# Performance work log

Hardware: AMD Instinct MI355X
Metric: run time of the kernel (lower is better)

Reference implementation:

```python
import jax, jax.numpy as jnp
import numpy as np

GRID_SIZE = 5       # efficient-KAN defaults
SPLINE_ORDER = 3
GRID_RANGE = (-1.0, 1.0)
N_BASIS = GRID_SIZE + SPLINE_ORDER  # 8
LN_EPS = 1e-5


def _make_grid(in_features):
    h = (GRID_RANGE[1] - GRID_RANGE[0]) / GRID_SIZE
    g = np.arange(-SPLINE_ORDER, GRID_SIZE + SPLINE_ORDER + 1, dtype=np.float32) * h + GRID_RANGE[0]
    return jnp.asarray(np.tile(g, (in_features, 1)))  # [in, G+2k+1]


def _b_splines(x, grid):
    # x: [N, in], grid: [in, G+2k+1] -> [N, in, G+k]
    x = x[..., None]
    bases = ((x >= grid[:, :-1]) & (x < grid[:, 1:])).astype(x.dtype)
    for k in range(1, SPLINE_ORDER + 1):
        bases = ((x - grid[:, : -(k + 1)]) / (grid[:, k:-1] - grid[:, : -(k + 1)]) * bases[..., :-1]
                 + (grid[:, k + 1:] - x) / (grid[:, k + 1:] - grid[:, 1:-k]) * bases[..., 1:])
    return bases


def _layer_norm(x, scale, bias):
    mu = jnp.mean(x, axis=-1, keepdims=True)
    var = jnp.mean(jnp.square(x - mu), axis=-1, keepdims=True)
    return (x - mu) * jax.lax.rsqrt(var + LN_EPS) * scale + bias


def setup_inputs() -> dict:
    key = jax.random.key(0)
    B, S, D = 2, 4096, 256
    IN = 3 * D
    ks = jax.random.split(key, 20)
    s = 0.02
    inp = {
        'axial_tokens': jax.random.normal(ks[0], (B, S, D), jnp.float32),
        'sagittal_tokens': jax.random.normal(ks[1], (B, S, D), jnp.float32),
        'coronal_tokens': jax.random.normal(ks[2], (B, S, D), jnp.float32),
        'wq': jax.random.normal(ks[3], (D, D), jnp.float32) * s,
        'bq': jnp.zeros((D,), jnp.float32),
        'wk': jax.random.normal(ks[4], (D, D), jnp.float32) * s,
        'bk': jnp.zeros((D,), jnp.float32),
        'wv': jax.random.normal(ks[5], (D, D), jnp.float32) * s,
        'bv': jnp.zeros((D,), jnp.float32),
        'view_emb': jax.random.normal(ks[6], (3, D), jnp.float32) * s,
        'ln_ax_scale': jnp.ones((D,), jnp.float32), 'ln_ax_bias': jnp.zeros((D,), jnp.float32),
        'ln_sg_scale': jnp.ones((D,), jnp.float32), 'ln_sg_bias': jnp.zeros((D,), jnp.float32),
        'ln_co_scale': jnp.ones((D,), jnp.float32), 'ln_co_bias': jnp.zeros((D,), jnp.float32),
        'base_weight': jax.random.normal(ks[7], (D, IN), jnp.float32) * s,
        'spline_weight': jax.random.normal(ks[8], (D, IN, N_BASIS), jnp.float32) * s,
        'spline_scaler': 1.0 + jax.random.normal(ks[9], (D, IN), jnp.float32) * 0.1,
    }
    return inp


def reference(axial_tokens, sagittal_tokens, coronal_tokens,
              wq, bq, wk, bk, wv, bv, view_emb,
              ln_ax_scale, ln_ax_bias, ln_sg_scale, ln_sg_bias, ln_co_scale, ln_co_bias,
              base_weight, spline_weight, spline_scaler):
    D = axial_tokens.shape[-1]
    inv_sqrt_d = 1.0 / jnp.sqrt(jnp.float32(D))

    def attend(tokens, emb, ln_s, ln_b):
        q = tokens @ wq.T + bq
        k = tokens @ wk.T + bk
        v = tokens @ wv.T + bv
        # torch adds q @ view_emb_row_broadcast^T: every column of the bias equals q . emb
        bias = (q @ emb)[..., None]                      # [B,S,1]
        scores = jnp.einsum('bqd,bkd->bqk', q, k) * inv_sqrt_d + bias
        w = jax.nn.softmax(scores, axis=-1)
        att = jnp.einsum('bqk,bkd->bqd', w, v)
        return _layer_norm(att + tokens, ln_s, ln_b)

    ax = attend(axial_tokens, view_emb[0], ln_ax_scale, ln_ax_bias)
    sg = attend(sagittal_tokens, view_emb[1], ln_sg_scale, ln_sg_bias)
    co = attend(coronal_tokens, view_emb[2], ln_co_scale, ln_co_bias)

    x = jnp.concatenate((ax, sg, co), axis=-1)          # [B,S,3D]
    B, S, IN = x.shape
    grid = _make_grid(IN)
    base = jax.nn.silu(x) @ base_weight.T               # [B,S,D]
    sb = _b_splines(x.reshape(-1, IN), grid)            # [B*S, IN, G+k]
    sw = spline_weight * spline_scaler[..., None]       # [D, IN, G+k]
    spline = jnp.einsum('nif,oif->no', sb, sw).reshape(B, S, -1)
    return base + spline
```

## Files before the change

### kernel.cpp

```cpp
#include <hip/hip_runtime.h>
#include <hip/hip_bf16.h>
#include <math.h>


typedef __hip_bfloat16 bf16;
using bf16x8 = __attribute__((ext_vector_type(8))) __bf16;
using f32x4  = __attribute__((ext_vector_type(4))) float;

__device__ __forceinline__ void load_lds16(const void* g, void* l) {
  __builtin_amdgcn_global_load_lds((__attribute__((address_space(1))) void*)g,
                                   (__attribute__((address_space(3))) void*)l,
                                   16, 0, 0);
}

__device__ __forceinline__ float wave_sum(float v) {
#pragma unroll
  for (int o = 32; o > 0; o >>= 1) v += __shfl_down(v, o, 64);
  return v;
}

template <typename OutT, bool EXP>
__global__ __launch_bounds__(256) void mfma_gemm_bt(
    const bf16* __restrict__ A, const bf16* __restrict__ B,
    const float* __restrict__ bias, OutT* __restrict__ C, int K, int lda,
    int ldb, int ldc, size_t zAh, size_t zAl, size_t zBh, size_t zBl,
    size_t zC, float scale) {
  __shared__ __align__(16) bf16 As[4096];
  __shared__ __align__(16) bf16 Bs[4096];
  const int tid = (int)threadIdx.x;
  const int lane = tid & 63;
  const int w = tid >> 6;
  const int m0 = (int)blockIdx.y << 7;
  const int n0 = (int)blockIdx.x << 7;
  const size_t z = blockIdx.z;
  A += (z >> 1) * zAh + (z & 1) * zAl;
  B += (z >> 1) * zBh + (z & 1) * zBl;
  C += z * zC;

  const int srow = lane >> 2;
  const int qg = (lane & 3) ^ ((lane >> 3) & 3);
  const int ci0 = w, ci1 = w + 4;
  const bf16* gA0 = A + (size_t)(m0 + ci0 * 16 + srow) * lda + qg * 8;
  const bf16* gA1 = A + (size_t)(m0 + ci1 * 16 + srow) * lda + qg * 8;
  const bf16* gB0 = B + (size_t)(n0 + ci0 * 16 + srow) * ldb + qg * 8;
  const bf16* gB1 = B + (size_t)(n0 + ci1 * 16 + srow) * ldb + qg * 8;
  bf16* lA0 = As + ci0 * 512;
  bf16* lA1 = As + ci1 * 512;
  bf16* lB0 = Bs + ci0 * 512;
  bf16* lB1 = Bs + ci1 * 512;

  const int m15 = lane & 15, quad = lane >> 4;
  const int fq = quad ^ ((m15 >> 1) & 3);
  const int aoff = m15 * 32 + fq * 8;
  const bf16* pA = As + ((w >> 1) << 11) + aoff;
  const bf16* pB = Bs + ((w & 1) << 11) + aoff;

  f32x4 acc[4][4];
#pragma unroll
  for (int mi = 0; mi < 4; ++mi)
#pragma unroll
    for (int ni = 0; ni < 4; ++ni) acc[mi][ni] = (f32x4)(0.0f);

  for (int k0 = 0; k0 < K; k0 += 32) {
    load_lds16(gA0, lA0);
    load_lds16(gA1, lA1);
    load_lds16(gB0, lB0);
    load_lds16(gB1, lB1);
    gA0 += 32; gA1 += 32; gB0 += 32; gB1 += 32;
    __syncthreads();
    bf16x8 av[4], bv[4];
#pragma unroll
    for (int i = 0; i < 4; ++i) {
      av[i] = *(const bf16x8*)(pA + i * 512);
      bv[i] = *(const bf16x8*)(pB + i * 512);
    }
#pragma unroll
    for (int mi = 0; mi < 4; ++mi)
#pragma unroll
      for (int ni = 0; ni < 4; ++ni)
        acc[mi][ni] = __builtin_amdgcn_mfma_f32_16x16x32_bf16(
            av[mi], bv[ni], acc[mi][ni], 0, 0, 0);
    __syncthreads();
  }

  const int crow = m0 + ((w >> 1) << 6) + quad * 4;
  const int ccol = n0 + ((w & 1) << 6) + m15;
#pragma unroll
  for (int ni = 0; ni < 4; ++ni) {
    const int col = ccol + ni * 16;
    const float bb = bias ? bias[col] : 0.0f;
#pragma unroll
    for (int mi = 0; mi < 4; ++mi) {
#pragma unroll
      for (int i = 0; i < 4; ++i) {
        const int row = crow + mi * 16 + i;
        float v = acc[mi][ni][i] * scale + bb;
        if constexpr (EXP) v = __expf(v);
        if constexpr (sizeof(OutT) == 2)
          C[(size_t)row * ldc + col] = __float2bfloat16(v);
        else
          C[(size_t)row * ldc + col] = v;
      }
    }
  }
}

__global__ __launch_bounds__(256) void rowsum_kernel(
    const bf16* __restrict__ P, float* __restrict__ l) {
  __shared__ float red[4];
  const int tid = (int)threadIdx.x;
  const bf16* p = P + (size_t)blockIdx.x * 4096 + tid * 16;
  float s = 0.f;
#pragma unroll
  for (int t = 0; t < 16; ++t) s += __bfloat162float(p[t]);
  s = wave_sum(s);
  if ((tid & 63) == 0) red[tid >> 6] = s;
  __syncthreads();
  if (tid == 0) l[blockIdx.x] = red[0] + red[1] + red[2] + red[3];
}

__global__ __launch_bounds__(256) void resid_ln_kernel(
    const float* __restrict__ attp, const float* __restrict__ l,
    const float* __restrict__ tok, const float* __restrict__ gamma,
    const float* __restrict__ beta, float* __restrict__ x, int vIdx) {
  __shared__ float red[4];
  const int n = (int)blockIdx.x;
  const int d = (int)threadIdx.x;
  const int b = n >> 12, r = n & 4095;
  const size_t base = ((size_t)(b * 2) * 4096 + r) * 256 + d;
  const float a0 = attp[base];
  const float a1 = attp[base + (size_t)4096 * 256];
  const float invl = 1.0f / l[b * 4096 + r];
  const float y = (a0 + a1) * invl + tok[(size_t)n * 256 + d];
  float s = wave_sum(y);
  if ((d & 63) == 0) red[d >> 6] = s;
  __syncthreads();
  const float mu = (red[0] + red[1] + red[2] + red[3]) * (1.0f / 256.0f);
  __syncthreads();
  const float c = y - mu;
  float s2 = wave_sum(c * c);
  if ((d & 63) == 0) red[d >> 6] = s2;
  __syncthreads();
  const float var = (red[0] + red[1] + red[2] + red[3]) * (1.0f / 256.0f);
  const float rs = rsqrtf(var + 1e-5f);
  x[(size_t)n * 768 + vIdx * 256 + d] = c * rs * gamma[d] + beta[d];
}

__global__ __launch_bounds__(256) void prep_w(
    const float* __restrict__ bw, const float* __restrict__ sw,
    const float* __restrict__ scaler, bf16* __restrict__ Wmat) {
  const int o = blockIdx.x;
  for (int ii = 0; ii < 3; ++ii) {
    const int i = ii * 256 + (int)threadIdx.x;
    const float s = scaler[(size_t)o * 768 + i];
    bf16* p = Wmat + (size_t)o * 7680 + i * 10;
    const float* swp = sw + ((size_t)o * 768 + i) * 8;
#pragma unroll
    for (int f = 0; f < 8; ++f) p[f] = __float2bfloat16(swp[f] * s);
    const bf16 bwb = __float2bfloat16(bw[(size_t)o * 768 + i]);
    p[8] = bwb;
    p[9] = bwb;
  }
}

__global__ __launch_bounds__(256) void prep_qkvw(
    const float* __restrict__ wq, const float* __restrict__ wk,
    const float* __restrict__ wv, const float* __restrict__ bq,
    const float* __restrict__ bk, const float* __restrict__ bv,
    bf16* __restrict__ wqkvb, float* __restrict__ bqkv) {
  const int idx = blockIdx.x * 256 + (int)threadIdx.x;
  const int row = idx >> 8, col = idx & 255;
  const float* src = row < 256 ? wq : (row < 512 ? wk : wv);
  wqkvb[idx] = __float2bfloat16(src[((row & 255) << 8) + col]);
  if (idx < 768)
    bqkv[idx] = idx < 256 ? bq[idx] : (idx < 512 ? bk[idx - 256] : bv[idx - 512]);
}

__global__ __launch_bounds__(256) void cast_tok3(
    const float4* __restrict__ t0, const float4* __restrict__ t1,
    const float4* __restrict__ t2, bf16* __restrict__ dst) {
  const int vv = blockIdx.y;
  const float4* src = vv == 0 ? t0 : (vv == 1 ? t1 : t2);
  const int idx = blockIdx.x * 256 + (int)threadIdx.x;
  const float4 val = src[idx];
  bf16* p = dst + (size_t)vv * 2097152 + (size_t)idx * 4;
  p[0] = __float2bfloat16(val.x);
  p[1] = __float2bfloat16(val.y);
  p[2] = __float2bfloat16(val.z);
  p[3] = __float2bfloat16(val.w);
}

__global__ __launch_bounds__(256) void transpose_v(
    const bf16* __restrict__ qkv, bf16* __restrict__ vT) {
  __shared__ bf16 tle[64][65];
  const int s0 = blockIdx.x << 6, d0 = blockIdx.y << 6, z = blockIdx.z;
  const int tid = (int)threadIdx.x;
  const int c = tid & 63, rr = tid >> 6;
  for (int r = 0; r < 64; r += 4)
    tle[r + rr][c] = qkv[(size_t)(z * 4096 + s0 + r + rr) * 768 + 512 + d0 + c];
  __syncthreads();
  for (int r = 0; r < 64; r += 4)
    vT[(size_t)z * 1048576 + (size_t)(d0 + r + rr) * 4096 + s0 + c] =
        tle[c][r + rr];
}

__global__ __launch_bounds__(256) void basis_kernel(
    const float* __restrict__ x, bf16* __restrict__ basis) {
  const int i = blockIdx.x * 256 + (int)threadIdx.x;
  const int n = blockIdx.y;
  const float xv = x[(size_t)n * 768 + i];
  float b[11];
#pragma unroll
  for (int m = 0; m < 11; ++m) {
    const float g0 = 0.4f * (float)(m - 3) - 1.0f;
    const float g1 = 0.4f * (float)(m - 2) - 1.0f;
    b[m] = (xv >= g0 && xv < g1) ? 1.0f : 0.0f;
  }
#pragma unroll
  for (int k = 1; k <= 3; ++k) {
    const float inv = 1.0f / (0.4f * (float)k);
#pragma unroll
    for (int m = 0; m + k < 11; ++m) {
      const float gm = 0.4f * (float)(m - 3) - 1.0f;
      const float gmk1 = 0.4f * (float)(m + k - 2) - 1.0f;
      b[m] = (xv - gm) * inv * b[m] + (gmk1 - xv) * inv * b[m + 1];
    }
  }
  bf16* p = basis + (size_t)n * 7680 + i * 10;
#pragma unroll
  for (int f = 0; f < 8; ++f) p[f] = __float2bfloat16(b[f]);
  const float sil = xv / (1.0f + __expf(-xv));
  const bf16 hi = __float2bfloat16(sil);
  p[8] = hi;
  p[9] = __float2bfloat16(sil - __bfloat162float(hi));
}

__global__ __launch_bounds__(256) void combine_kernel(
    const float4* __restrict__ p0, const float4* __restrict__ p1,
    float4* __restrict__ out) {
  const int idx = blockIdx.x * 256 + (int)threadIdx.x;
  const float4 a = p0[idx], b = p1[idx];
  out[idx] = make_float4(a.x + b.x, a.y + b.y, a.z + b.z, a.w + b.w);
}

extern "C" void kernel_launch(void* const* d_in, const int* in_sizes, int n_in,
                              void* d_out, int out_size, void* d_ws,
                              size_t ws_size, hipStream_t stream) {
  const float* tok[3] = {(const float*)d_in[0], (const float*)d_in[1],
                         (const float*)d_in[2]};
  const float* wq = (const float*)d_in[3];
  const float* bq = (const float*)d_in[4];
  const float* wk = (const float*)d_in[5];
  const float* bk = (const float*)d_in[6];
  const float* wv = (const float*)d_in[7];
  const float* bv = (const float*)d_in[8];
  const float* lng[3] = {(const float*)d_in[10], (const float*)d_in[12],
                         (const float*)d_in[14]};
  const float* lnb[3] = {(const float*)d_in[11], (const float*)d_in[13],
                         (const float*)d_in[15]};
  const float* bw = (const float*)d_in[16];
  const float* sw = (const float*)d_in[17];
  const float* scaler = (const float*)d_in[18];

  char* w8 = (char*)d_ws;
  bf16* tokb = (bf16*)(w8 + 0);
  bf16* qkv = (bf16*)(w8 + 12582912);
  bf16* vT = (bf16*)(w8 + 50331648);
  bf16* Pb = (bf16*)(w8 + 62914560);
  float* lrow = (float*)(w8 + 130023424);
  float* attp = (float*)(w8 + 130056192);
  float* x = (float*)(w8 + 146833408);
  bf16* Wmat = (bf16*)(w8 + 171999232);
  bf16* wqkvb = (bf16*)(w8 + 175931392);
  float* bqkv = (float*)(w8 + 176324608);
  float* pout = (float*)(w8 + 176327680);
  bf16* basis = (bf16*)(w8 + 0);

  prep_w<<<256, 256, 0, stream>>>(bw, sw, scaler, Wmat);
  prep_qkvw<<<768, 256, 0, stream>>>(wq, wk, wv, bq, bk, bv, wqkvb, bqkv);
  cast_tok3<<<dim3(2048, 3), 256, 0, stream>>>(
      (const float4*)tok[0], (const float4*)tok[1], (const float4*)tok[2],
      tokb);

  mfma_gemm_bt<bf16, false><<<dim3(6, 192, 1), 256, 0, stream>>>(
      tokb, wqkvb, bqkv, qkv, 256, 256, 256, 768, 0, 0, 0, 0, 0, 1.0f);
  transpose_v<<<dim3(64, 4, 6), 256, 0, stream>>>(qkv, vT);

  for (int v = 0; v < 3; ++v) {
    for (int b = 0; b < 2; ++b) {
      const bf16* qb = qkv + (size_t)(2 * v + b) * 4096 * 768;
      mfma_gemm_bt<bf16, true><<<dim3(32, 32, 1), 256, 0, stream>>>(
          qb, qb + 256, nullptr, Pb + (size_t)b * 16777216, 256, 768, 768,
          4096, 0, 0, 0, 0, 0, 0.0625f);
      rowsum_kernel<<<4096, 256, 0, stream>>>(Pb + (size_t)b * 16777216,
                                              lrow + b * 4096);
    }
    mfma_gemm_bt<float, false><<<dim3(2, 32, 4), 256, 0, stream>>>(
        Pb, vT + (size_t)(2 * v) * 1048576, nullptr, attp, 2048, 4096, 4096,
        256, 16777216, 2048, 1048576, 2048, 1048576, 1.0f);
    resid_ln_kernel<<<8192, 256, 0, stream>>>(attp, lrow, tok[v], lng[v],
                                              lnb[v], x, v);
  }

  basis_kernel<<<dim3(3, 8192), 256, 0, stream>>>(x, basis);
  mfma_gemm_bt<float, false><<<dim3(2, 64, 2), 256, 0, stream>>>(
      basis, Wmat, nullptr, pout, 3840, 7680, 7680, 256, 0, 3840, 0, 3840,
      2097152, 1.0f);
  combine_kernel<<<2048, 256, 0, stream>>>(
      (const float4*)pout, (const float4*)(pout + (size_t)8192 * 256),
      (float4*)d_out);
}
```

Before: 606.3 us.

## Fuse softmax row sums into score GEMM and raise split-K for PV and KAN GEMMs

The exp-score GEMM epilogue now reduces per-row partial sums across lanes and writes them to a partial buffer, which removes the separate rowsum kernel that re-read the large probability matrix. The PV GEMM and the final KAN GEMM move from 2-way to 4-way split-K, and the LN and combine kernels sum four partials. The KAN basis layout shrinks from 10 to 9 columns per feature by dropping the hi/lo split of the SiLU term, which cuts K and memory traffic. The SiLU path loses the extra precision that split carried, and the added partial writes and reads cost more memory traffic.

```diff
diff --git a/kernel.cpp b/kernel.cpp
--- a/kernel.cpp
+++ b/kernel.cpp
@@ -22,9 +22,9 @@
 template <typename OutT, bool EXP>
 __global__ __launch_bounds__(256) void mfma_gemm_bt(
     const bf16* __restrict__ A, const bf16* __restrict__ B,
-    const float* __restrict__ bias, OutT* __restrict__ C, int K, int lda,
-    int ldb, int ldc, size_t zAh, size_t zAl, size_t zBh, size_t zBl,
-    size_t zC, float scale) {
+    const float* __restrict__ bias, OutT* __restrict__ C,
+    float* __restrict__ lpart, int K, int lda, int ldb, int ldc, int zshift,
+    size_t zAh, size_t zAl, size_t zBh, size_t zBl, size_t zC, float scale) {
   __shared__ __align__(16) bf16 As[4096];
   __shared__ __align__(16) bf16 Bs[4096];
   const int tid = (int)threadIdx.x;
@@ -33,8 +33,9 @@
   const int m0 = (int)blockIdx.y << 7;
   const int n0 = (int)blockIdx.x << 7;
   const size_t z = blockIdx.z;
-  A += (z >> 1) * zAh + (z & 1) * zAl;
-  B += (z >> 1) * zBh + (z & 1) * zBl;
+  const size_t zlo = z & (((size_t)1 << zshift) - 1);
+  A += (z >> zshift) * zAh + zlo * zAl;
+  B += (z >> zshift) * zBh + zlo * zBl;
   C += z * zC;
 
   const int srow = lane >> 2;
@@ -85,6 +86,7 @@
 
   const int crow = m0 + ((w >> 1) << 6) + quad * 4;
   const int ccol = n0 + ((w & 1) << 6) + m15;
+  float rs[4][4] = {};
 #pragma unroll
   for (int ni = 0; ni < 4; ++ni) {
     const int col = ccol + ni * 16;
@@ -95,7 +97,10 @@
       for (int i = 0; i < 4; ++i) {
         const int row = crow + mi * 16 + i;
         float v = acc[mi][ni][i] * scale + bb;
-        if constexpr (EXP) v = __expf(v);
+        if constexpr (EXP) {
+          v = __expf(v);
+          rs[mi][i] += v;
+        }
         if constexpr (sizeof(OutT) == 2)
           C[(size_t)row * ldc + col] = __float2bfloat16(v);
         else
@@ -103,35 +108,41 @@
       }
     }
   }
-}
-
-__global__ __launch_bounds__(256) void rowsum_kernel(
-    const bf16* __restrict__ P, float* __restrict__ l) {
-  __shared__ float red[4];
-  const int tid = (int)threadIdx.x;
-  const bf16* p = P + (size_t)blockIdx.x * 4096 + tid * 16;
-  float s = 0.f;
-#pragma unroll
-  for (int t = 0; t < 16; ++t) s += __bfloat162float(p[t]);
-  s = wave_sum(s);
-  if ((tid & 63) == 0) red[tid >> 6] = s;
-  __syncthreads();
-  if (tid == 0) l[blockIdx.x] = red[0] + red[1] + red[2] + red[3];
+  if constexpr (EXP) {
+    const int ch = ((int)blockIdx.x << 1) | (w & 1);
+#pragma unroll
+    for (int mi = 0; mi < 4; ++mi)
+#pragma unroll
+      for (int i = 0; i < 4; ++i) {
+        float sv = rs[mi][i];
+        sv += __shfl_xor(sv, 1);
+        sv += __shfl_xor(sv, 2);
+        sv += __shfl_xor(sv, 4);
+        sv += __shfl_xor(sv, 8);
+        if (m15 == 0)
+          lpart[(size_t)ch * 4096 + crow + mi * 16 + i] = sv;
+      }
+  }
 }
 
 __global__ __launch_bounds__(256) void resid_ln_kernel(
-    const float* __restrict__ attp, const float* __restrict__ l,
+    const float* __restrict__ attp, const float* __restrict__ lpart,
     const float* __restrict__ tok, const float* __restrict__ gamma,
     const float* __restrict__ beta, float* __restrict__ x, int vIdx) {
   __shared__ float red[4];
+  __shared__ float sinvl;
   const int n = (int)blockIdx.x;
   const int d = (int)threadIdx.x;
   const int b = n >> 12, r = n & 4095;
-  const size_t base = ((size_t)(b * 2) * 4096 + r) * 256 + d;
-  const float a0 = attp[base];
-  const float a1 = attp[base + (size_t)4096 * 256];
-  const float invl = 1.0f / l[b * 4096 + r];
-  const float y = (a0 + a1) * invl + tok[(size_t)n * 256 + d];
+  float ls = 0.f;
+  if (d < 64) ls = lpart[((size_t)(b * 64 + d)) * 4096 + r];
+  ls = wave_sum(ls);
+  if (d == 0) sinvl = 1.0f / ls;
+  const size_t abase = (size_t)(b * 4) * 1048576 + (size_t)r * 256 + d;
+  const float asum = attp[abase] + attp[abase + 1048576] +
+                     attp[abase + 2097152] + attp[abase + 3145728];
+  __syncthreads();
+  const float y = asum * sinvl + tok[(size_t)n * 256 + d];
   float s = wave_sum(y);
   if ((d & 63) == 0) red[d >> 6] = s;
   __syncthreads();
@@ -142,8 +153,8 @@
   if ((d & 63) == 0) red[d >> 6] = s2;
   __syncthreads();
   const float var = (red[0] + red[1] + red[2] + red[3]) * (1.0f / 256.0f);
-  const float rs = rsqrtf(var + 1e-5f);
-  x[(size_t)n * 768 + vIdx * 256 + d] = c * rs * gamma[d] + beta[d];
+  const float rstd = rsqrtf(var + 1e-5f);
+  x[(size_t)n * 768 + vIdx * 256 + d] = c * rstd * gamma[d] + beta[d];
 }
 
 __global__ __launch_bounds__(256) void prep_w(
@@ -153,13 +164,11 @@
   for (int ii = 0; ii < 3; ++ii) {
     const int i = ii * 256 + (int)threadIdx.x;
     const float s = scaler[(size_t)o * 768 + i];
-    bf16* p = Wmat + (size_t)o * 7680 + i * 10;
+    bf16* p = Wmat + (size_t)o * 6912 + i * 9;
     const float* swp = sw + ((size_t)o * 768 + i) * 8;
 #pragma unroll
     for (int f = 0; f < 8; ++f) p[f] = __float2bfloat16(swp[f] * s);
-    const bf16 bwb = __float2bfloat16(bw[(size_t)o * 768 + i]);
-    p[8] = bwb;
-    p[9] = bwb;
+    p[8] = __float2bfloat16(bw[(size_t)o * 768 + i]);
   }
 }
 
@@ -226,21 +235,22 @@
       b[m] = (xv - gm) * inv * b[m] + (gmk1 - xv) * inv * b[m + 1];
     }
   }
-  bf16* p = basis + (size_t)n * 7680 + i * 10;
+  bf16* p = basis + (size_t)n * 6912 + i * 9;
 #pragma unroll
   for (int f = 0; f < 8; ++f) p[f] = __float2bfloat16(b[f]);
-  const float sil = xv / (1.0f + __expf(-xv));
-  const bf16 hi = __float2bfloat16(sil);
-  p[8] = hi;
-  p[9] = __float2bfloat16(sil - __bfloat162float(hi));
-}
-
-__global__ __launch_bounds__(256) void combine_kernel(
-    const float4* __restrict__ p0, const float4* __restrict__ p1,
-    float4* __restrict__ out) {
+  p[8] = __float2bfloat16(xv / (1.0f + __expf(-xv)));
+}
+
+__global__ __launch_bounds__(256) void combine4_kernel(
+    const float4* __restrict__ p, float4* __restrict__ out) {
   const int idx = blockIdx.x * 256 + (int)threadIdx.x;
-  const float4 a = p0[idx], b = p1[idx];
-  out[idx] = make_float4(a.x + b.x, a.y + b.y, a.z + b.z, a.w + b.w);
+  const float4 a = p[idx];
+  const float4 b = p[idx + 524288];
+  const float4 c = p[idx + 1048576];
+  const float4 d = p[idx + 1572864];
+  out[idx] =
+      make_float4(a.x + b.x + c.x + d.x, a.y + b.y + c.y + d.y,
+                  a.z + b.z + c.z + d.z, a.w + b.w + c.w + d.w);
 }
 
 extern "C" void kernel_launch(void* const* d_in, const int* in_sizes, int n_in,
@@ -267,14 +277,14 @@
   bf16* qkv = (bf16*)(w8 + 12582912);
   bf16* vT = (bf16*)(w8 + 50331648);
   bf16* Pb = (bf16*)(w8 + 62914560);
-  float* lrow = (float*)(w8 + 130023424);
-  float* attp = (float*)(w8 + 130056192);
-  float* x = (float*)(w8 + 146833408);
-  bf16* Wmat = (bf16*)(w8 + 171999232);
-  bf16* wqkvb = (bf16*)(w8 + 175931392);
-  float* bqkv = (float*)(w8 + 176324608);
-  float* pout = (float*)(w8 + 176327680);
+  float* lpart = (float*)(w8 + 130023424);
+  float* attp = (float*)(w8 + 132120576);
+  float* x = (float*)(w8 + 165675008);
+  bf16* Wmat = (bf16*)(w8 + 190840832);
+  bf16* wqkvb = (bf16*)(w8 + 194379776);
+  float* bqkv = (float*)(w8 + 194772992);
   bf16* basis = (bf16*)(w8 + 0);
+  float* pout = attp;
 
   prep_w<<<256, 256, 0, stream>>>(bw, sw, scaler, Wmat);
   prep_qkvw<<<768, 256, 0, stream>>>(wq, wk, wv, bq, bk, bv, wqkvb, bqkv);
@@ -283,30 +293,29 @@
       tokb);
 
   mfma_gemm_bt<bf16, false><<<dim3(6, 192, 1), 256, 0, stream>>>(
-      tokb, wqkvb, bqkv, qkv, 256, 256, 256, 768, 0, 0, 0, 0, 0, 1.0f);
+      tokb, wqkvb, bqkv, qkv, nullptr, 256, 256, 256, 768, 1, 0, 0, 0, 0, 0,
+      1.0f);
   transpose_v<<<dim3(64, 4, 6), 256, 0, stream>>>(qkv, vT);
 
   for (int v = 0; v < 3; ++v) {
     for (int b = 0; b < 2; ++b) {
       const bf16* qb = qkv + (size_t)(2 * v + b) * 4096 * 768;
       mfma_gemm_bt<bf16, true><<<dim3(32, 32, 1), 256, 0, stream>>>(
-          qb, qb + 256, nullptr, Pb + (size_t)b * 16777216, 256, 768, 768,
-          4096, 0, 0, 0, 0, 0, 0.0625f);
-      rowsum_kernel<<<4096, 256, 0, stream>>>(Pb + (size_t)b * 16777216,
-                                              lrow + b * 4096);
+          qb, qb + 256, nullptr, Pb + (size_t)b * 16777216,
+          lpart + (size_t)b * 262144, 256, 768, 768, 4096, 1, 0, 0, 0, 0, 0,
+          0.0625f);
     }
-    mfma_gemm_bt<float, false><<<dim3(2, 32, 4), 256, 0, stream>>>(
-        Pb, vT + (size_t)(2 * v) * 1048576, nullptr, attp, 2048, 4096, 4096,
-        256, 16777216, 2048, 1048576, 2048, 1048576, 1.0f);
-    resid_ln_kernel<<<8192, 256, 0, stream>>>(attp, lrow, tok[v], lng[v],
+    mfma_gemm_bt<float, false><<<dim3(2, 32, 8), 256, 0, stream>>>(
+        Pb, vT + (size_t)(2 * v) * 1048576, nullptr, attp, nullptr, 1024,
+        4096, 4096, 256, 2, 16777216, 1024, 1048576, 1024, 1048576, 1.0f);
+    resid_ln_kernel<<<8192, 256, 0, stream>>>(attp, lpart, tok[v], lng[v],
                                               lnb[v], x, v);
   }
 
   basis_kernel<<<dim3(3, 8192), 256, 0, stream>>>(x, basis);
-  mfma_gemm_bt<float, false><<<dim3(2, 64, 2), 256, 0, stream>>>(
-      basis, Wmat, nullptr, pout, 3840, 7680, 7680, 256, 0, 3840, 0, 3840,
-      2097152, 1.0f);
-  combine_kernel<<<2048, 256, 0, stream>>>(
-      (const float4*)pout, (const float4*)(pout + (size_t)8192 * 256),
-      (float4*)d_out);
-}
+  mfma_gemm_bt<float, false><<<dim3(2, 64, 4), 256, 0, stream>>>(
+      basis, Wmat, nullptr, pout, nullptr, 1728, 6912, 6912, 256, 2, 0, 1728,
+      0, 1728, 2097152, 1.0f);
+  combine4_kernel<<<2048, 256, 0, stream>>>((const float4*)pout,
+                                            (float4*)d_out);
+}
```

Measured after the change: 544.7 us. 10.2% less time.
